# Performance work log

Hardware: AMD Instinct MI355X
Metric: run time of the kernel (lower is better)

Reference implementation:

```python
import jax, jax.numpy as jnp
import numpy as np

SLIDING_WINDOW = 512  # matches init kwarg
BLOCK_STRIDE = 32     # tokens per cache page


def setup_inputs() -> dict:
    key = jax.random.key(0)
    k0, k1, k2, k3 = jax.random.split(key, 4)
    B, S, HQ, HKV, D = 2, 2048, 32, 8, 128
    nb = S // BLOCK_STRIDE
    q = jax.random.normal(k0, (B, S, HQ, D), jnp.float32)
    k = jax.random.normal(k1, (B, S, HKV, D), jnp.float32)
    v = jax.random.normal(k2, (B, S, HKV, D), jnp.float32)
    sink = jax.random.normal(k3, (HQ,), jnp.float32)
    cache_state = jnp.zeros((B * nb, 2, HKV, BLOCK_STRIDE, D), jnp.float32)
    seq_block_ids = jnp.arange(B * nb, dtype=jnp.int32).reshape(B, nb)
    return {"q": q, "k": k, "v": v, "cache_state": cache_state,
            "seq_block_ids": seq_block_ids, "sink": sink}


def reference(q, k, v, cache_state, seq_block_ids, sink):
    B, S, HQ, D = q.shape
    HKV = k.shape[2]
    G = HQ // HKV  # GQA group size
    stride = cache_state.shape[3]
    nb = S // stride

    # --- write prefill K/V into the paged cache ---
    # pages laid out [num_pages, k/v, HKV, stride, D]
    k_pg = k.reshape(B, nb, stride, HKV, D).transpose(0, 1, 3, 2, 4).reshape(B * nb, HKV, stride, D)
    v_pg = v.reshape(B, nb, stride, HKV, D).transpose(0, 1, 3, 2, 4).reshape(B * nb, HKV, stride, D)
    ids = seq_block_ids.reshape(-1)
    new_cache = cache_state.at[ids, 0].set(k_pg).at[ids, 1].set(v_pg)

    # --- sliding-window causal attention with sink logits (GQA, no repeat) ---
    scale = 1.0 / np.sqrt(D).astype(np.float32)
    qg = q.reshape(B, S, HKV, G, D)
    # scores: [B, HKV, G, Sq, Sk]
    scores = jnp.einsum('bqhgd,bshd->bhgqs', qg, k) * scale
    i = jnp.arange(S)[:, None]
    j = jnp.arange(S)[None, :]
    allowed = (j <= i) & ((i - j) < SLIDING_WINDOW)  # causal banded mask
    neg = jnp.finfo(scores.dtype).min
    scores = jnp.where(allowed, scores, neg)
    # per-head sink logit appended as extra key column, dropped after softmax
    sink_col = jnp.broadcast_to(sink.reshape(HKV, G)[None, :, :, None, None], (B, HKV, G, S, 1))
    probs = jax.nn.softmax(jnp.concatenate([scores, sink_col], axis=-1), axis=-1)[..., :S]
    out = jnp.einsum('bhgqs,bshd->bqhgd', probs, v).reshape(B, S, HQ, D)
    return out, new_cache
```

## Files before the change

### kernel.cpp

```cpp
#include <hip/hip_runtime.h>
#include <hip/hip_bf16.h>
#include <stdint.h>

#define BB 2
#define SS 2048
#define HQ 32
#define HKV 8
#define DD 128
#define WIN 512

typedef __bf16 bf16x8 __attribute__((ext_vector_type(8)));
typedef __bf16 bf16x4 __attribute__((ext_vector_type(4)));
typedef float f32x4 __attribute__((ext_vector_type(4)));

__device__ __forceinline__ bf16x8 cvt8(float4 a, float4 b, float s) {
  bf16x8 r;
  r[0] = (__bf16)(a.x * s); r[1] = (__bf16)(a.y * s);
  r[2] = (__bf16)(a.z * s); r[3] = (__bf16)(a.w * s);
  r[4] = (__bf16)(b.x * s); r[5] = (__bf16)(b.y * s);
  r[6] = (__bf16)(b.z * s); r[7] = (__bf16)(b.w * s);
  return r;
}

__global__ __launch_bounds__(512, 2) void attn_kernel(
    const float* __restrict__ qg, const float* __restrict__ kg,
    const float* __restrict__ vg, const float* __restrict__ sinkg,
    float* __restrict__ outg)
{
  const int col = (blockIdx.x & 7) + 8 * ((blockIdx.x >> 3) & 1);
  const int rank = blockIdx.x >> 4;
  const int qtile = rank < 24 ? rank + 8 : 31 - rank;
  const int hkv = col & 7, b = col >> 3;
  const int qb = qtile * 64;
  const int tid = threadIdx.x;
  const int wave = tid >> 6, lane = tid & 63;
  const int wq = wave & 3, wh = wave >> 2;
  const int g = lane >> 4, c = lane & 15;
  const int hq0 = (hkv << 2) + (wh << 1);

  __shared__ __bf16 Kl[2][32 * 128];
  __shared__ __bf16 Vt[2][128 * 40];
  __shared__ __bf16 Pl[16][16 * 40];

  const float LOG2E = 1.4426950408889634f;
  const float scale = 0.08838834764831845f * LOG2E;
  const float THR = 12.0f;
  const int qw = qb + wq * 16;
  const int qrow = qw + c;

  bf16x8 qf[2][4];
  #pragma unroll
  for (int hh = 0; hh < 2; ++hh) {
    const float* qp = qg + (((size_t)b * SS + qrow) * HQ + hq0 + hh) * DD;
    #pragma unroll
    for (int ch = 0; ch < 4; ++ch) {
      float4 a = *(const float4*)(qp + ch * 32 + g * 8);
      float4 b2 = *(const float4*)(qp + ch * 32 + g * 8 + 4);
      qf[hh][ch] = cvt8(a, b2, scale);
    }
  }

  const float sk[2] = {sinkg[hq0] * LOG2E, sinkg[hq0 + 1] * LOG2E};

  float mm[2] = {-1e30f, -1e30f}, ll[2] = {0.f, 0.f};
  f32x4 acc[2][8];
  #pragma unroll
  for (int hh = 0; hh < 2; ++hh)
    #pragma unroll
    for (int i = 0; i < 8; ++i) acc[hh][i] = (f32x4){0.f, 0.f, 0.f, 0.f};

  const int t0 = (qb > (WIN - 1) ? (qb - (WIN - 1)) : 0) >> 5;
  const int t1 = (qb + 63) >> 5;

  const int krow = tid >> 4, kh = tid & 15;
  const int vd = tid & 127, vc4 = tid >> 7;
  const int KSTEP = 32 * HKV * DD;
  const float* kp = kg + (((size_t)b * SS + (t0 << 5) + krow) * HKV + hkv) * DD + kh * 8;
  const float* vp = vg + (((size_t)b * SS + (t0 << 5) + vc4 * 8) * HKV + hkv) * DD + vd;

  float4 ka, ka2; float vr[8];
  auto issue = [&]() {
    ka = *(const float4*)(kp);
    ka2 = *(const float4*)(kp + 4);
    #pragma unroll
    for (int j = 0; j < 8; ++j) vr[j] = vp[(size_t)j * (HKV * DD)];
  };
  auto commit = [&](int buf) {
    *(bf16x8*)((char*)(&Kl[buf][0]) + krow * 256 + ((kh * 16) ^ ((krow & 7) << 4))) =
        cvt8(ka, ka2, 1.f);
    bf16x8 w;
    #pragma unroll
    for (int j = 0; j < 8; ++j) w[j] = (__bf16)vr[j];
    *(bf16x8*)(&Vt[buf][vd * 40 + vc4 * 8]) = w;
  };

  issue();
  commit(0);
  __syncthreads();
  int cur = 0;

  for (int t = t0; t <= t1; ++t) {
    const int kb = t << 5;
    const bool hn = (t < t1);
    if (hn) { kp += KSTEP; vp += KSTEP; issue(); }

    const bool active = !(kb > qw + 15 || kb + 31 < qw - (WIN - 1));
    if (active) {
      const __bf16* Ks = &Kl[cur][0];
      const __bf16* Vs = &Vt[cur][0];

      f32x4 s0[2] = {{0.f,0.f,0.f,0.f},{0.f,0.f,0.f,0.f}};
      f32x4 s1[2] = {{0.f,0.f,0.f,0.f},{0.f,0.f,0.f,0.f}};
      __builtin_amdgcn_s_setprio(1);
      #pragma unroll
      for (int ch = 0; ch < 4; ++ch) {
        const int off = (ch * 64 + g * 16) ^ ((c & 7) << 4);
        bf16x8 a0 = *(const bf16x8*)((const char*)Ks + c * 256 + off);
        bf16x8 a1 = *(const bf16x8*)((const char*)Ks + (16 + c) * 256 + off);
        s0[0] = __builtin_amdgcn_mfma_f32_16x16x32_bf16(a0, qf[0][ch], s0[0], 0, 0, 0);
        s1[0] = __builtin_amdgcn_mfma_f32_16x16x32_bf16(a1, qf[0][ch], s1[0], 0, 0, 0);
        s0[1] = __builtin_amdgcn_mfma_f32_16x16x32_bf16(a0, qf[1][ch], s0[1], 0, 0, 0);
        s1[1] = __builtin_amdgcn_mfma_f32_16x16x32_bf16(a1, qf[1][ch], s1[1], 0, 0, 0);
      }
      __builtin_amdgcn_s_setprio(0);

      const bool noMask = (kb + 31 <= qw) && (kb >= qw - (WIN - 16));

      #pragma unroll
      for (int hh = 0; hh < 2; ++hh) {
        float p[8];
        #pragma unroll
        for (int r = 0; r < 4; ++r) { p[r] = s0[hh][r]; p[4 + r] = s1[hh][r]; }
        if (!noMask) {
          #pragma unroll
          for (int t2 = 0; t2 < 2; ++t2)
            #pragma unroll
            for (int r = 0; r < 4; ++r) {
              const int kk = kb + t2 * 16 + g * 4 + r;
              const bool ok = (kk <= qrow) && (qrow - kk < WIN);
              p[t2 * 4 + r] = ok ? p[t2 * 4 + r] : -1e30f;
            }
        }
        float tmax = p[0];
        #pragma unroll
        for (int j = 1; j < 8; ++j) tmax = fmaxf(tmax, p[j]);
        tmax = fmaxf(tmax, __shfl_xor(tmax, 16));
        tmax = fmaxf(tmax, __shfl_xor(tmax, 32));

        const bool resc = __any(tmax > mm[hh] + THR);
        const float mnew = resc ? fmaxf(mm[hh], tmax) : mm[hh];
        float tsum = 0.f;
        if (noMask) {
          #pragma unroll
          for (int j = 0; j < 8; ++j) { p[j] = exp2f(p[j] - mnew); tsum += p[j]; }
        } else {
          #pragma unroll
          for (int j = 0; j < 8; ++j) {
            const float e = (p[j] > -9e29f) ? exp2f(p[j] - mnew) : 0.f;
            p[j] = e; tsum += e;
          }
        }
        tsum += __shfl_xor(tsum, 16);
        tsum += __shfl_xor(tsum, 32);

        if (resc) {
          const float scl = exp2f(mm[hh] - mnew);
          ll[hh] = ll[hh] * scl + tsum;
          #pragma unroll
          for (int dt = 0; dt < 8; ++dt) {
            acc[hh][dt][0] *= scl; acc[hh][dt][1] *= scl;
            acc[hh][dt][2] *= scl; acc[hh][dt][3] *= scl;
          }
          mm[hh] = mnew;
        } else {
          ll[hh] += tsum;
        }

        char* pb = (char*)(&Pl[wave * 2 + hh][0]) + c * 80;
        #pragma unroll
        for (int t2 = 0; t2 < 2; ++t2) {
          bf16x4 w;
          w[0] = (__bf16)p[t2 * 4 + 0]; w[1] = (__bf16)p[t2 * 4 + 1];
          w[2] = (__bf16)p[t2 * 4 + 2]; w[3] = (__bf16)p[t2 * 4 + 3];
          *(bf16x4*)(pb + t2 * 32 + g * 8) = w;
        }
      }

      bf16x8 pa0 = *(bf16x8*)((char*)(&Pl[wave * 2 + 0][0]) + c * 80 + g * 16);
      bf16x8 pa1 = *(bf16x8*)((char*)(&Pl[wave * 2 + 1][0]) + c * 80 + g * 16);
      __builtin_amdgcn_s_setprio(1);
      #pragma unroll
      for (int dt = 0; dt < 8; ++dt) {
        bf16x8 vv = *(const bf16x8*)(Vs + (dt * 16 + c) * 40 + g * 8);
        acc[0][dt] = __builtin_amdgcn_mfma_f32_16x16x32_bf16(vv, pa0, acc[0][dt], 0, 0, 0);
        acc[1][dt] = __builtin_amdgcn_mfma_f32_16x16x32_bf16(vv, pa1, acc[1][dt], 0, 0, 0);
      }
      __builtin_amdgcn_s_setprio(0);
    }

    if (hn) {
      commit(cur ^ 1);
      __syncthreads();
      cur ^= 1;
    }
  }

  #pragma unroll
  for (int hh = 0; hh < 2; ++hh) {
    const float Mf = fmaxf(mm[hh], sk[hh]);
    const float ex = exp2f(mm[hh] - Mf);
    const float denom = ll[hh] * ex + exp2f(sk[hh] - Mf);
    const float fac = ex / denom;
    float* orow = outg + (((size_t)b * SS + qw + c) * HQ + hq0 + hh) * DD;
    #pragma unroll
    for (int dt = 0; dt < 8; ++dt) {
      float4 o;
      o.x = acc[hh][dt][0] * fac; o.y = acc[hh][dt][1] * fac;
      o.z = acc[hh][dt][2] * fac; o.w = acc[hh][dt][3] * fac;
      *(float4*)(orow + dt * 16 + 4 * g) = o;
    }
  }
}

__global__ void build_inv(const int* __restrict__ ids, int* __restrict__ inv,
                          int npages, int nslots) {
  const int i = threadIdx.x;
  if (i < npages) inv[i] = -1;
  __syncthreads();
  if (i < nslots) inv[ids[i]] = i;
}

__global__ void page_fill(const float* __restrict__ kg, const float* __restrict__ vg,
                          const float* __restrict__ cache_in, const int* __restrict__ inv,
                          float* __restrict__ cache) {
  const int page = blockIdx.x, half = blockIdx.y;
  const int slot = inv[page];
  float4* d4 = (float4*)cache;
  const size_t dbase = (((size_t)page * 2 + half) * 8) * 1024;
  if (slot >= 0) {
    const int b = slot >> 6, blk = slot & 63;
    const float4* s4 = (const float4*)(half ? vg : kg);
    for (int f = threadIdx.x; f < 8192; f += blockDim.x) {
      const int d = f & 31, s = (f >> 5) & 31, h = f >> 10;
      d4[dbase + (size_t)h * 1024 + s * 32 + d] =
          s4[(((size_t)b * SS + blk * 32 + s) * 8 + h) * 32 + d];
    }
  } else {
    const float4* s4 = (const float4*)cache_in;
    for (int f = threadIdx.x; f < 8192; f += blockDim.x)
      d4[dbase + f] = s4[dbase + f];
  }
}

__global__ void cache_copy(const float* __restrict__ src, float* __restrict__ dst, int n4) {
  const float4* s = (const float4*)src;
  float4* d = (float4*)dst;
  for (int i = blockIdx.x * blockDim.x + threadIdx.x; i < n4; i += gridDim.x * blockDim.x)
    d[i] = s[i];
}
__global__ void cache_scatter(const float* __restrict__ kg, const float* __restrict__ vg,
                              const int* __restrict__ ids, float* __restrict__ cache) {
  const int slot = blockIdx.x;
  const int half = blockIdx.y;
  const int b = slot >> 6, blk = slot & 63;
  const int page = ids[slot];
  const float4* s4 = (const float4*)(half ? vg : kg);
  float4* d4 = (float4*)cache;
  for (int f = threadIdx.x; f < 8192; f += blockDim.x) {
    const int d = f & 31, s = (f >> 5) & 31, h = f >> 10;
    d4[(((size_t)page * 2 + half) * 8 + h) * 1024 + s * 32 + d] =
        s4[(((size_t)b * SS + blk * 32 + s) * 8 + h) * 32 + d];
  }
}

extern "C" void kernel_launch(void* const* d_in, const int* in_sizes, int n_in,
                              void* d_out, int out_size, void* d_ws, size_t ws_size,
                              hipStream_t stream) {
  const float* q = (const float*)d_in[0];
  const float* k = (const float*)d_in[1];
  const float* v = (const float*)d_in[2];
  const float* cache_in = (const float*)d_in[3];
  const int* ids = (const int*)d_in[4];
  const float* sink = (const float*)d_in[5];
  float* out = (float*)d_out;
  float* cache_out = out + (size_t)BB * SS * HQ * DD;

  const int nslots = in_sizes[4];
  const int npages = in_sizes[3] / (2 * HKV * 32 * DD);

  if (ws_size >= (size_t)npages * sizeof(int) && npages <= 1024) {
    int* inv = (int*)d_ws;
    build_inv<<<1, 1024, 0, stream>>>(ids, inv, npages, nslots);
    page_fill<<<dim3(npages, 2), 256, 0, stream>>>(k, v, cache_in, inv, cache_out);
  } else {
    cache_copy<<<4096, 256, 0, stream>>>(cache_in, cache_out, (BB * SS * HKV * DD * 2) / 4);
    cache_scatter<<<dim3(BB * 64, 2), 256, 0, stream>>>(k, v, ids, cache_out);
  }
  attn_kernel<<<512, 512, 0, stream>>>(q, k, v, sink, out);
}
```

Measured before the change: 112.8 us.

## Switch attention to 32x32x16 MFMA with register-resident P and 64-key tiles

Restructures the attention kernel around 32x32x16 bf16 MFMA. Each wave now owns one query head and 32 query rows, and key/value tiles grow from 32 to 64 tokens with XOR-swizzled LDS layouts. The probability matrix no longer round-trips through LDS: it is packed with v_cvt_pk_bf16_f32 and exchanged across half-waves with shuffles. The per-wave tile-skip check is dropped. The intent is fewer LDS transactions and instructions and higher MFMA efficiency, at the cost of larger register and LDS footprint and some wasted work on fully masked tiles.

```diff
diff --git a/kernel.cpp b/kernel.cpp
--- a/kernel.cpp
+++ b/kernel.cpp
@@ -10,8 +10,7 @@
 #define WIN 512
 
 typedef __bf16 bf16x8 __attribute__((ext_vector_type(8)));
-typedef __bf16 bf16x4 __attribute__((ext_vector_type(4)));
-typedef float f32x4 __attribute__((ext_vector_type(4)));
+typedef float f32x16 __attribute__((ext_vector_type(16)));
 
 __device__ __forceinline__ bf16x8 cvt8(float4 a, float4 b, float s) {
   bf16x8 r;
@@ -20,6 +19,12 @@
   r[4] = (__bf16)(b.x * s); r[5] = (__bf16)(b.y * s);
   r[6] = (__bf16)(b.z * s); r[7] = (__bf16)(b.w * s);
   return r;
+}
+
+__device__ __forceinline__ uint32_t pk2(float lo, float hi) {
+  uint32_t w;
+  asm("v_cvt_pk_bf16_f32 %0, %1, %2" : "=v"(w) : "v"(lo), "v"(hi));
+  return w;
 }
 
 __global__ __launch_bounds__(512, 2) void attn_kernel(
@@ -34,190 +39,208 @@
   const int qb = qtile * 64;
   const int tid = threadIdx.x;
   const int wave = tid >> 6, lane = tid & 63;
-  const int wq = wave & 3, wh = wave >> 2;
-  const int g = lane >> 4, c = lane & 15;
-  const int hq0 = (hkv << 2) + (wh << 1);
-
-  __shared__ __bf16 Kl[2][32 * 128];
-  __shared__ __bf16 Vt[2][128 * 40];
-  __shared__ __bf16 Pl[16][16 * 40];
+  const int c5 = lane & 31, hi = lane >> 5;
+  const int hq = (hkv << 2) + (wave >> 1);
+  const int qw = qb + (wave & 1) * 32;
+  const int qrow = qw + c5;
+
+  __shared__ __align__(16) __bf16 Kl[2][64 * 128];
+  __shared__ __align__(16) __bf16 Vt[2][128 * 64];
 
   const float LOG2E = 1.4426950408889634f;
   const float scale = 0.08838834764831845f * LOG2E;
   const float THR = 12.0f;
-  const int qw = qb + wq * 16;
-  const int qrow = qw + c;
-
-  bf16x8 qf[2][4];
+
+  bf16x8 qf[8];
+  {
+    const float* qp = qg + (((size_t)b * SS + qrow) * HQ + hq) * DD + hi * 8;
+    #pragma unroll
+    for (int ch = 0; ch < 8; ++ch) {
+      float4 a = *(const float4*)(qp + ch * 16);
+      float4 a2 = *(const float4*)(qp + ch * 16 + 4);
+      qf[ch] = cvt8(a, a2, scale);
+    }
+  }
+  const float sk = sinkg[hq] * LOG2E;
+
+  float mm = -1e30f, ll = 0.f;
+  f32x16 acc[4];
   #pragma unroll
-  for (int hh = 0; hh < 2; ++hh) {
-    const float* qp = qg + (((size_t)b * SS + qrow) * HQ + hq0 + hh) * DD;
-    #pragma unroll
-    for (int ch = 0; ch < 4; ++ch) {
-      float4 a = *(const float4*)(qp + ch * 32 + g * 8);
-      float4 b2 = *(const float4*)(qp + ch * 32 + g * 8 + 4);
-      qf[hh][ch] = cvt8(a, b2, scale);
-    }
-  }
-
-  const float sk[2] = {sinkg[hq0] * LOG2E, sinkg[hq0 + 1] * LOG2E};
-
-  float mm[2] = {-1e30f, -1e30f}, ll[2] = {0.f, 0.f};
-  f32x4 acc[2][8];
-  #pragma unroll
-  for (int hh = 0; hh < 2; ++hh)
-    #pragma unroll
-    for (int i = 0; i < 8; ++i) acc[hh][i] = (f32x4){0.f, 0.f, 0.f, 0.f};
-
-  const int t0 = (qb > (WIN - 1) ? (qb - (WIN - 1)) : 0) >> 5;
-  const int t1 = (qb + 63) >> 5;
-
-  const int krow = tid >> 4, kh = tid & 15;
-  const int vd = tid & 127, vc4 = tid >> 7;
-  const int KSTEP = 32 * HKV * DD;
-  const float* kp = kg + (((size_t)b * SS + (t0 << 5) + krow) * HKV + hkv) * DD + kh * 8;
-  const float* vp = vg + (((size_t)b * SS + (t0 << 5) + vc4 * 8) * HKV + hkv) * DD + vd;
-
-  float4 ka, ka2; float vr[8];
-  auto issue = [&]() {
-    ka = *(const float4*)(kp);
-    ka2 = *(const float4*)(kp + 4);
-    #pragma unroll
-    for (int j = 0; j < 8; ++j) vr[j] = vp[(size_t)j * (HKV * DD)];
+  for (int d = 0; d < 4; ++d)
+    #pragma unroll
+    for (int r = 0; r < 16; ++r) acc[d][r] = 0.f;
+
+  const int t0 = (qb > (WIN - 1) ? (qb - (WIN - 1)) : 0) >> 6;
+  const int t1 = (qb + 63) >> 6;
+
+  const int krow = tid >> 3, kchunk = tid & 7;
+  const int vd = tid & 127, vslot = tid >> 7;
+  const size_t KSTEP = (size_t)64 * HKV * DD;
+  const float* kBase = kg + (((size_t)b * SS + krow) * HKV + hkv) * DD + kchunk * 16;
+  const float* vBase = vg + (((size_t)b * SS + vslot * 16) * HKV + hkv) * DD + vd;
+
+  float4 k0, k1, k2, k3; float vr[16];
+  auto issue = [&](int t) {
+    const float* kp = kBase + (size_t)t * KSTEP;
+    k0 = *(const float4*)(kp);     k1 = *(const float4*)(kp + 4);
+    k2 = *(const float4*)(kp + 8); k3 = *(const float4*)(kp + 12);
+    const float* vp = vBase + (size_t)t * KSTEP;
+    #pragma unroll
+    for (int j = 0; j < 16; ++j) vr[j] = vp[(size_t)j * (HKV * DD)];
   };
+  const int ksw = ((krow ^ (krow >> 3)) & 7) << 4;
+  const int vsw = ((vd ^ (vd >> 3)) & 7) << 4;
   auto commit = [&](int buf) {
-    *(bf16x8*)((char*)(&Kl[buf][0]) + krow * 256 + ((kh * 16) ^ ((krow & 7) << 4))) =
-        cvt8(ka, ka2, 1.f);
-    bf16x8 w;
-    #pragma unroll
-    for (int j = 0; j < 8; ++j) w[j] = (__bf16)vr[j];
-    *(bf16x8*)(&Vt[buf][vd * 40 + vc4 * 8]) = w;
+    char* kd = (char*)(&Kl[buf][0]) + krow * 256;
+    *(bf16x8*)(kd + ((kchunk * 32) ^ ksw)) = cvt8(k0, k1, 1.f);
+    *(bf16x8*)(kd + ((kchunk * 32 + 16) ^ ksw)) = cvt8(k2, k3, 1.f);
+    char* vdst = (char*)(&Vt[buf][0]) + vd * 128;
+    bf16x8 w0, w1;
+    #pragma unroll
+    for (int j = 0; j < 8; ++j) { w0[j] = (__bf16)vr[j]; w1[j] = (__bf16)vr[8 + j]; }
+    *(bf16x8*)(vdst + ((vslot * 32) ^ vsw)) = w0;
+    *(bf16x8*)(vdst + ((vslot * 32 + 16) ^ vsw)) = w1;
   };
 
-  issue();
+  issue(t0);
   commit(0);
   __syncthreads();
   int cur = 0;
 
+  const int swA = ((c5 ^ (c5 >> 3)) & 7) << 4;
+  const int swB = swA ^ 0x40;
+
   for (int t = t0; t <= t1; ++t) {
-    const int kb = t << 5;
-    const bool hn = (t < t1);
-    if (hn) { kp += KSTEP; vp += KSTEP; issue(); }
-
-    const bool active = !(kb > qw + 15 || kb + 31 < qw - (WIN - 1));
-    if (active) {
-      const __bf16* Ks = &Kl[cur][0];
-      const __bf16* Vs = &Vt[cur][0];
-
-      f32x4 s0[2] = {{0.f,0.f,0.f,0.f},{0.f,0.f,0.f,0.f}};
-      f32x4 s1[2] = {{0.f,0.f,0.f,0.f},{0.f,0.f,0.f,0.f}};
-      __builtin_amdgcn_s_setprio(1);
-      #pragma unroll
-      for (int ch = 0; ch < 4; ++ch) {
-        const int off = (ch * 64 + g * 16) ^ ((c & 7) << 4);
-        bf16x8 a0 = *(const bf16x8*)((const char*)Ks + c * 256 + off);
-        bf16x8 a1 = *(const bf16x8*)((const char*)Ks + (16 + c) * 256 + off);
-        s0[0] = __builtin_amdgcn_mfma_f32_16x16x32_bf16(a0, qf[0][ch], s0[0], 0, 0, 0);
-        s1[0] = __builtin_amdgcn_mfma_f32_16x16x32_bf16(a1, qf[0][ch], s1[0], 0, 0, 0);
-        s0[1] = __builtin_amdgcn_mfma_f32_16x16x32_bf16(a0, qf[1][ch], s0[1], 0, 0, 0);
-        s1[1] = __builtin_amdgcn_mfma_f32_16x16x32_bf16(a1, qf[1][ch], s1[1], 0, 0, 0);
-      }
-      __builtin_amdgcn_s_setprio(0);
-
-      const bool noMask = (kb + 31 <= qw) && (kb >= qw - (WIN - 16));
-
-      #pragma unroll
-      for (int hh = 0; hh < 2; ++hh) {
-        float p[8];
+    if (t < t1) issue(t + 1);
+    const int kb = t << 6;
+    const char* Ksc = (const char*)&Kl[cur][0];
+    const char* Vsc = (const char*)&Vt[cur][0];
+
+    f32x16 s0, s1;
+    #pragma unroll
+    for (int r = 0; r < 16; ++r) { s0[r] = 0.f; s1[r] = 0.f; }
+    __builtin_amdgcn_s_setprio(1);
+    #pragma unroll
+    for (int ch = 0; ch < 8; ++ch) {
+      const int colb = ch * 32 + hi * 16;
+      bf16x8 a0 = *(const bf16x8*)(Ksc + c5 * 256 + (colb ^ swA));
+      bf16x8 a1 = *(const bf16x8*)(Ksc + (32 + c5) * 256 + (colb ^ swB));
+      s0 = __builtin_amdgcn_mfma_f32_32x32x16_bf16(a0, qf[ch], s0, 0, 0, 0);
+      s1 = __builtin_amdgcn_mfma_f32_32x32x16_bf16(a1, qf[ch], s1, 0, 0, 0);
+    }
+    __builtin_amdgcn_s_setprio(0);
+
+    const bool noMask = (kb + 63 <= qw) && (kb >= qw - (WIN - 32));
+
+    if (!noMask) {
+      #pragma unroll
+      for (int r = 0; r < 16; ++r) {
+        const int lr = (r & 3) + 8 * (r >> 2) + 4 * hi;
+        const int kv0 = kb + lr, kv1 = kv0 + 32;
+        const bool ok0 = (kv0 <= qrow) && (qrow - kv0 < WIN);
+        const bool ok1 = (kv1 <= qrow) && (qrow - kv1 < WIN);
+        s0[r] = ok0 ? s0[r] : -1e30f;
+        s1[r] = ok1 ? s1[r] : -1e30f;
+      }
+    }
+    float tmax = s0[0];
+    #pragma unroll
+    for (int r = 1; r < 16; ++r) tmax = fmaxf(tmax, s0[r]);
+    #pragma unroll
+    for (int r = 0; r < 16; ++r) tmax = fmaxf(tmax, s1[r]);
+    tmax = fmaxf(tmax, __shfl_xor(tmax, 32));
+
+    const bool resc = __any(tmax > mm + THR);
+    const float mnew = resc ? fmaxf(mm, tmax) : mm;
+    float tsum = 0.f;
+    if (noMask) {
+      #pragma unroll
+      for (int r = 0; r < 16; ++r) {
+        s0[r] = exp2f(s0[r] - mnew); tsum += s0[r];
+        s1[r] = exp2f(s1[r] - mnew); tsum += s1[r];
+      }
+    } else {
+      #pragma unroll
+      for (int r = 0; r < 16; ++r) {
+        s0[r] = (s0[r] > -9e29f) ? exp2f(s0[r] - mnew) : 0.f; tsum += s0[r];
+        s1[r] = (s1[r] > -9e29f) ? exp2f(s1[r] - mnew) : 0.f; tsum += s1[r];
+      }
+    }
+    tsum += __shfl_xor(tsum, 32);
+
+    if (resc) {
+      const float scl = exp2f(mm - mnew);
+      ll = ll * scl + tsum;
+      #pragma unroll
+      for (int d = 0; d < 4; ++d)
         #pragma unroll
-        for (int r = 0; r < 4; ++r) { p[r] = s0[hh][r]; p[4 + r] = s1[hh][r]; }
-        if (!noMask) {
-          #pragma unroll
-          for (int t2 = 0; t2 < 2; ++t2)
-            #pragma unroll
-            for (int r = 0; r < 4; ++r) {
-              const int kk = kb + t2 * 16 + g * 4 + r;
-              const bool ok = (kk <= qrow) && (qrow - kk < WIN);
-              p[t2 * 4 + r] = ok ? p[t2 * 4 + r] : -1e30f;
-            }
-        }
-        float tmax = p[0];
-        #pragma unroll
-        for (int j = 1; j < 8; ++j) tmax = fmaxf(tmax, p[j]);
-        tmax = fmaxf(tmax, __shfl_xor(tmax, 16));
-        tmax = fmaxf(tmax, __shfl_xor(tmax, 32));
-
-        const bool resc = __any(tmax > mm[hh] + THR);
-        const float mnew = resc ? fmaxf(mm[hh], tmax) : mm[hh];
-        float tsum = 0.f;
-        if (noMask) {
-          #pragma unroll
-          for (int j = 0; j < 8; ++j) { p[j] = exp2f(p[j] - mnew); tsum += p[j]; }
-        } else {
-          #pragma unroll
-          for (int j = 0; j < 8; ++j) {
-            const float e = (p[j] > -9e29f) ? exp2f(p[j] - mnew) : 0.f;
-            p[j] = e; tsum += e;
-          }
-        }
-        tsum += __shfl_xor(tsum, 16);
-        tsum += __shfl_xor(tsum, 32);
-
-        if (resc) {
-          const float scl = exp2f(mm[hh] - mnew);
-          ll[hh] = ll[hh] * scl + tsum;
-          #pragma unroll
-          for (int dt = 0; dt < 8; ++dt) {
-            acc[hh][dt][0] *= scl; acc[hh][dt][1] *= scl;
-            acc[hh][dt][2] *= scl; acc[hh][dt][3] *= scl;
-          }
-          mm[hh] = mnew;
-        } else {
-          ll[hh] += tsum;
-        }
-
-        char* pb = (char*)(&Pl[wave * 2 + hh][0]) + c * 80;
-        #pragma unroll
-        for (int t2 = 0; t2 < 2; ++t2) {
-          bf16x4 w;
-          w[0] = (__bf16)p[t2 * 4 + 0]; w[1] = (__bf16)p[t2 * 4 + 1];
-          w[2] = (__bf16)p[t2 * 4 + 2]; w[3] = (__bf16)p[t2 * 4 + 3];
-          *(bf16x4*)(pb + t2 * 32 + g * 8) = w;
-        }
-      }
-
-      bf16x8 pa0 = *(bf16x8*)((char*)(&Pl[wave * 2 + 0][0]) + c * 80 + g * 16);
-      bf16x8 pa1 = *(bf16x8*)((char*)(&Pl[wave * 2 + 1][0]) + c * 80 + g * 16);
-      __builtin_amdgcn_s_setprio(1);
-      #pragma unroll
-      for (int dt = 0; dt < 8; ++dt) {
-        bf16x8 vv = *(const bf16x8*)(Vs + (dt * 16 + c) * 40 + g * 8);
-        acc[0][dt] = __builtin_amdgcn_mfma_f32_16x16x32_bf16(vv, pa0, acc[0][dt], 0, 0, 0);
-        acc[1][dt] = __builtin_amdgcn_mfma_f32_16x16x32_bf16(vv, pa1, acc[1][dt], 0, 0, 0);
-      }
-      __builtin_amdgcn_s_setprio(0);
-    }
-
-    if (hn) {
+        for (int r = 0; r < 16; ++r) acc[d][r] *= scl;
+      mm = mnew;
+    } else {
+      ll += tsum;
+    }
+
+    bf16x8 pb[4];
+    #pragma unroll
+    for (int kvq = 0; kvq < 4; ++kvq) {
+      const int bq = (kvq & 1) * 8;
+      float e0, e1, e2, e3, e4, e5, e6, e7;
+      if (kvq & 2) {
+        e0 = s1[bq+0]; e1 = s1[bq+1]; e2 = s1[bq+2]; e3 = s1[bq+3];
+        e4 = s1[bq+4]; e5 = s1[bq+5]; e6 = s1[bq+6]; e7 = s1[bq+7];
+      } else {
+        e0 = s0[bq+0]; e1 = s0[bq+1]; e2 = s0[bq+2]; e3 = s0[bq+3];
+        e4 = s0[bq+4]; e5 = s0[bq+5]; e6 = s0[bq+6]; e7 = s0[bq+7];
+      }
+      const uint32_t A0 = pk2(e0, e1), A1 = pk2(e2, e3);
+      const uint32_t B0 = pk2(e4, e5), B1 = pk2(e6, e7);
+      const uint32_t XA0 = __shfl_xor(A0, 32), XA1 = __shfl_xor(A1, 32);
+      const uint32_t XB0 = __shfl_xor(B0, 32), XB1 = __shfl_xor(B1, 32);
+      union { uint4 u; bf16x8 v; } cvu;
+      cvu.u.x = hi ? XB0 : A0;
+      cvu.u.y = hi ? XB1 : A1;
+      cvu.u.z = hi ? B0 : XA0;
+      cvu.u.w = hi ? B1 : XA1;
+      pb[kvq] = cvu.v;
+    }
+
+    __builtin_amdgcn_s_setprio(1);
+    #pragma unroll
+    for (int d = 0; d < 4; ++d) {
+      const int rowb = (d * 32 + c5) * 128;
+      const int swV = swA ^ ((d & 1) << 6);
+      #pragma unroll
+      for (int kvq = 0; kvq < 4; ++kvq) {
+        bf16x8 va = *(const bf16x8*)(Vsc + rowb + ((kvq * 32 + hi * 16) ^ swV));
+        acc[d] = __builtin_amdgcn_mfma_f32_32x32x16_bf16(va, pb[kvq], acc[d], 0, 0, 0);
+      }
+    }
+    __builtin_amdgcn_s_setprio(0);
+
+    if (t < t1) {
       commit(cur ^ 1);
       __syncthreads();
       cur ^= 1;
     }
   }
 
-  #pragma unroll
-  for (int hh = 0; hh < 2; ++hh) {
-    const float Mf = fmaxf(mm[hh], sk[hh]);
-    const float ex = exp2f(mm[hh] - Mf);
-    const float denom = ll[hh] * ex + exp2f(sk[hh] - Mf);
+  {
+    const float Mf = fmaxf(mm, sk);
+    const float ex = exp2f(mm - Mf);
+    const float denom = ll * ex + exp2f(sk - Mf);
     const float fac = ex / denom;
-    float* orow = outg + (((size_t)b * SS + qw + c) * HQ + hq0 + hh) * DD;
-    #pragma unroll
-    for (int dt = 0; dt < 8; ++dt) {
-      float4 o;
-      o.x = acc[hh][dt][0] * fac; o.y = acc[hh][dt][1] * fac;
-      o.z = acc[hh][dt][2] * fac; o.w = acc[hh][dt][3] * fac;
-      *(float4*)(orow + dt * 16 + 4 * g) = o;
+    float* orow = outg + (((size_t)b * SS + qrow) * HQ + hq) * DD;
+    #pragma unroll
+    for (int d = 0; d < 4; ++d) {
+      #pragma unroll
+      for (int q4 = 0; q4 < 4; ++q4) {
+        float4 o;
+        o.x = acc[d][q4 * 4 + 0] * fac;
+        o.y = acc[d][q4 * 4 + 1] * fac;
+        o.z = acc[d][q4 * 4 + 2] * fac;
+        o.w = acc[d][q4 * 4 + 3] * fac;
+        *(float4*)(orow + d * 32 + q4 * 8 + 4 * hi) = o;
+      }
     }
   }
 }
```

New measurement: 108.4 us. 3.9% less time.
